# Kernel optimization log

Measured on AMD Instinct MI355X. Metric: run time of the kernel, lower is better.

The kernel has to match this reference:

```python
import jax, jax.numpy as jnp
import numpy as np
from jax import lax

VOCAB = 28996  # bert-base-cased vocab size (static for segment_sum)
B, S, D = 32, 512, 768
NUM_CLASSES = 9


def _lstm_dir(x, w_ih, w_hh, b_ih, b_hh):
    # x: [T, N, In]; torch gate order i, f, g, o packed along dim 0 of weights
    T, N, _ = x.shape
    H = w_hh.shape[1]
    xg = jnp.einsum('tni,gi->tng', x, w_ih) + b_ih  # precompute input projections [T,N,4H]

    def step(carry, xg_t):
        h, c = carry
        g = xg_t + h @ w_hh.T + b_hh
        i, f, gg, o = jnp.split(g, 4, axis=-1)
        c = jax.nn.sigmoid(f) * c + jax.nn.sigmoid(i) * jnp.tanh(gg)
        h = jax.nn.sigmoid(o) * jnp.tanh(c)
        return (h, c), h

    h0 = jnp.zeros((N, H), x.dtype)
    _, ys = lax.scan(step, (h0, h0), xg)
    return ys  # [T, N, H]


def setup_inputs() -> dict:
    key = jax.random.key(0)
    ks = jax.random.split(key, 8)
    H, In = D, 2 * D
    w = 0.02
    return {
        'batch': jax.random.randint(ks[0], (B, S), 0, VOCAB),
        'hidden': jax.random.normal(ks[1], (B, S, D), jnp.float32),
        'w_ih_f': jax.random.normal(ks[2], (4 * H, In), jnp.float32) * w,
        'w_hh_f': jax.random.normal(ks[3], (4 * H, H), jnp.float32) * w,
        'b_ih_f': jnp.zeros((4 * H,), jnp.float32),
        'b_hh_f': jnp.zeros((4 * H,), jnp.float32),
        'w_ih_b': jax.random.normal(ks[4], (4 * H, In), jnp.float32) * w,
        'w_hh_b': jax.random.normal(ks[5], (4 * H, H), jnp.float32) * w,
        'b_ih_b': jnp.zeros((4 * H,), jnp.float32),
        'b_hh_b': jnp.zeros((4 * H,), jnp.float32),
        'lin_w': jax.random.normal(ks[6], (NUM_CLASSES, 2 * H), jnp.float32) * w,
        'lin_b': jnp.zeros((NUM_CLASSES,), jnp.float32),
    }


def reference(batch, hidden, w_ih_f, w_hh_f, b_ih_f, b_hh_f,
              w_ih_b, w_hh_b, b_ih_b, b_hh_b, lin_w, lin_b):
    b, s, d = hidden.shape
    flat_ids = batch.reshape(-1)            # [B*S]
    flat_h = hidden.reshape(-1, d)          # [B*S, D]
    # segment mean of embeddings grouped by raw token id (the dict loop in torch)
    sums = jax.ops.segment_sum(flat_h, flat_ids, num_segments=VOCAB)
    counts = jax.ops.segment_sum(jnp.ones((flat_ids.shape[0], 1), hidden.dtype),
                                 flat_ids, num_segments=VOCAB)
    means = sums / jnp.maximum(counts, 1.0)
    ctx = means[flat_ids].reshape(b, s, d)  # gather-broadcast back per position
    x = jnp.concatenate([hidden, ctx], axis=2)  # [B, S, 2D]
    # nn.LSTM is not batch_first: scans over dim0 (B acts as time, S as batch)
    out_f = _lstm_dir(x, w_ih_f, w_hh_f, b_ih_f, b_hh_f)
    out_b = _lstm_dir(x[::-1], w_ih_b, w_hh_b, b_ih_b, b_hh_b)[::-1]
    out = jnp.concatenate([out_f, out_b], axis=-1)  # [B, S, 2D]
    # dropout is identity in eval mode
    return out @ lin_w.T + lin_b  # [B, S, num_classes]
```

## Files before the change

### kernel.cpp

```cpp
#include <hip/hip_runtime.h>

#define VOCAB 28996
#define BB 32
#define SS 512
#define DD 768
#define NCLS 9
#define ROWS (BB*SS)
#define IN2 (2*DD)
#define G4 (4*DD)
#define NB2 (2*G4)

typedef __attribute__((ext_vector_type(8))) short short8;
typedef __attribute__((ext_vector_type(4))) short shortx4;
typedef __attribute__((ext_vector_type(4))) float floatx4;
typedef unsigned long long ull;

__device__ __forceinline__ float bf2f(unsigned short u){
  union { unsigned int i; float f; } v; v.i = ((unsigned int)u) << 16; return v.f;
}
__device__ __forceinline__ unsigned short f2bf(float f){
  union { float f; unsigned int i; } v; v.f = f;
  unsigned int r = v.i + 0x7FFFu + ((v.i >> 16) & 1u);
  return (unsigned short)(r >> 16);
}
__device__ __forceinline__ float sigf(float x){ return 1.0f / (1.0f + __expf(-x)); }
__device__ __forceinline__ float tanhfast(float x){
  float y = fminf(fmaxf(x, -15.f), 15.f);
  float e = __expf(2.f * y);
  return 1.f - 2.f / (e + 1.f);
}

__device__ __forceinline__ void gl_lds16(const unsigned short* g, unsigned short* l){
  __builtin_amdgcn_global_load_lds((__attribute__((address_space(1))) void*)(g),
                                   (__attribute__((address_space(3))) void*)(l), 16, 0, 0);
}
__device__ __forceinline__ void gl_lds16_c(const unsigned short* g, unsigned short* l){
  __builtin_amdgcn_global_load_lds((__attribute__((address_space(1))) void*)(g),
                                   (__attribute__((address_space(3))) void*)(l), 16, 0, 17);
}
__device__ __forceinline__ void store16_sc1(unsigned short* p, short8 v){
  asm volatile("global_store_dwordx4 %0, %1, off sc0 sc1" :: "v"(p), "v"(v) : "memory");
}

__device__ __forceinline__ void grid_bar(unsigned* bar, int nb)
{
  __syncthreads();
  if (threadIdx.x == 0) {
    unsigned g = __hip_atomic_load(bar + 1, __ATOMIC_RELAXED, __HIP_MEMORY_SCOPE_AGENT);
    unsigned a = __hip_atomic_fetch_add(bar, 1u, __ATOMIC_RELAXED, __HIP_MEMORY_SCOPE_AGENT);
    if (a == (unsigned)(nb - 1)) {
      __hip_atomic_store(bar, 0u, __ATOMIC_RELAXED, __HIP_MEMORY_SCOPE_AGENT);
      __hip_atomic_store(bar + 1, g + 1u, __ATOMIC_RELEASE, __HIP_MEMORY_SCOPE_AGENT);
    } else {
      unsigned cur;
      do {
        __builtin_amdgcn_s_sleep(2);
        cur = __hip_atomic_load(bar + 1, __ATOMIC_RELAXED, __HIP_MEMORY_SCOPE_AGENT);
      } while (cur == g);
    }
  }
  __syncthreads();
}

__global__ void seg_scatter(const int* __restrict__ ids, const float* __restrict__ hidden,
                            float* __restrict__ sums, float* __restrict__ counts)
{
  int r = blockIdx.x;
  int id = ids[r];
  const float* h = hidden + (long)r * DD;
  float* s = sums + (long)id * DD;
  for (int d = threadIdx.x; d < DD; d += 256)
    atomicAdd(&s[d], h[d]);
  if (threadIdx.x == 0) atomicAdd(&counts[id], 1.0f);
}

__global__ void build_x(const int* __restrict__ ids, const float* __restrict__ hidden,
                        const float* __restrict__ sums, const float* __restrict__ counts,
                        unsigned short* __restrict__ x)
{
  int r = blockIdx.x;
  int id = ids[r];
  float inv = 1.0f / fmaxf(counts[id], 1.0f);
  const float* h = hidden + (long)r * DD;
  const float* s = sums + (long)id * DD;
  unsigned short* xr = x + (long)r * IN2;
  for (int d = threadIdx.x; d < DD; d += 256) {
    xr[d]      = f2bf(h[d]);
    xr[DD + d] = f2bf(s[d] * inv);
  }
}

__global__ void conv_w_perm(const float* __restrict__ w, unsigned short* __restrict__ o, int K)
{
  long i = (long)blockIdx.x * 256 + threadIdx.x;
  if (i >= (long)G4 * K) return;
  int row = (int)(i / K); int k = (int)(i - (long)row * K);
  int u = row >> 2, g = row & 3;
  o[i] = f2bf(w[((long)(g * DD + u)) * K + k]);
}

__global__ void conv_bias_perm(const float* __restrict__ bif, const float* __restrict__ bhf,
                               const float* __restrict__ bib, const float* __restrict__ bhb,
                               float* __restrict__ o)
{
  int n = blockIdx.x * 256 + threadIdx.x;
  if (n >= NB2) return;
  int d = n / G4, rr = n - d * G4, u = rr >> 2, g = rr & 3;
  int s = g * DD + u;
  o[n] = d ? (bib[s] + bhb[s]) : (bif[s] + bhf[s]);
}

__global__ __launch_bounds__(256, 2)
void gemm_bt(const unsigned short* __restrict__ A, int lda,
             const unsigned short* __restrict__ B, int ldb,
             unsigned short* __restrict__ C, int ldc,
             const float* __restrict__ bias, int K)
{
  __shared__ unsigned short lA[128 * 32];
  __shared__ unsigned short lB[128 * 32];
  const int t = threadIdx.x;
  const int lane = t & 63;
  const int wv = t >> 6;
  const int wm = wv >> 1, wn = wv & 1;
  const int l15 = lane & 15, q = lane >> 4;
  const long m0 = (long)blockIdx.y * 128;
  const long n0 = (long)blockIdx.x * 128;
  const int rowS = t >> 2;
  const int kc = (((t & 3) ^ ((t >> 3) & 3))) * 8;
  const int qsw = (q ^ ((l15 >> 1) & 3)) * 8;
  const unsigned short* gA = A + (m0 + rowS) * lda + kc;
  const unsigned short* gB = B + (n0 + rowS) * ldb + kc;
  unsigned short* dA0 = lA + (wv << 9);
  unsigned short* dA1 = lA + 2048 + (wv << 9);
  unsigned short* dB0 = lB + (wv << 9);
  unsigned short* dB1 = lB + 2048 + (wv << 9);

  floatx4 acc[4][4];
  #pragma unroll
  for (int i = 0; i < 4; i++)
    #pragma unroll
    for (int j = 0; j < 4; j++)
      acc[i][j] = (floatx4){0.f, 0.f, 0.f, 0.f};

  const long a64 = (long)64 * lda;
  const long b64 = (long)64 * ldb;
  for (int kt = 0; kt < K; kt += 32) {
    gl_lds16(gA + kt,       dA0);
    gl_lds16(gA + a64 + kt, dA1);
    gl_lds16(gB + kt,       dB0);
    gl_lds16(gB + b64 + kt, dB1);
    __syncthreads();
    short8 af[4], bfr[4];
    #pragma unroll
    for (int i = 0; i < 4; i++)
      af[i] = *(const short8*)(lA + (wm * 64 + i * 16 + l15) * 32 + qsw);
    #pragma unroll
    for (int j = 0; j < 4; j++)
      bfr[j] = *(const short8*)(lB + (wn * 64 + j * 16 + l15) * 32 + qsw);
    #pragma unroll
    for (int i = 0; i < 4; i++)
      #pragma unroll
      for (int j = 0; j < 4; j++)
        acc[i][j] = __builtin_amdgcn_mfma_f32_16x16x32_bf16(af[i], bfr[j], acc[i][j], 0, 0, 0);
    __syncthreads();
  }

  #pragma unroll
  for (int i = 0; i < 4; i++) {
    #pragma unroll
    for (int j = 0; j < 4; j++) {
      const long mg = m0 + wm * 64 + i * 16 + q * 4;
      const long ng = n0 + wn * 64 + j * 16 + l15;
      const float bb = bias[ng];
      #pragma unroll
      for (int r = 0; r < 4; r++)
        C[(mg + r) * ldc + ng] = f2bf(acc[i][j][r] + bb);
    }
  }
}

__global__ __launch_bounds__(512, 1)
void lstm_persist(const unsigned short* __restrict__ xg, int ldxg,
                  const unsigned short* __restrict__ whh,
                  unsigned short* __restrict__ hbuf,
                  unsigned short* __restrict__ outc,
                  unsigned* bar,
                  int dir0, int ndir)
{
  __shared__ unsigned short bufA[16384];
  __shared__ unsigned short bufB[16384];
  __shared__ unsigned short xgs[2][16384];
  __shared__ unsigned short hout[128 * 40];

  const int bid = blockIdx.x;
  const int xcd = bid & 7;
  const int idx = bid >> 3;
  int dm, k3;
  if (ndir == 2) { dm = idx & 7; k3 = idx >> 3; }
  else           { dm = idx & 3; k3 = idx >> 2; }
  const int ld  = (ndir == 2) ? (dm & 1) : 0;
  const int dir = dir0 + ld;
  const int mt  = (ndir == 2) ? (dm >> 1) : dm;
  const int nt  = k3 * 8 + xcd;
  const int m0 = mt * 128, n0 = nt * 128;
  const int u0 = n0 >> 2;
  unsigned* gbar = bar + dm * 16;

  const int t0 = threadIdx.x;
  const int lane = t0 & 63;
  const int wv = t0 >> 6;
  const int wm = wv >> 1;
  const int wn = wv & 1;
  const int l15 = lane & 15, q = lane >> 4;
  const long ldoff = (ndir == 2 && ld == 1) ? (long)G4 : 0;

  const unsigned short* Bdir = whh + (long)dir * G4 * DD;
  const int srow  = lane >> 2;
  const int scolA = (((lane & 3) ^ ((lane >> 3) & 3))) * 8;
  const int qsw   = (q ^ ((l15 >> 1) & 3)) * 8;
  const int xsw   = l15 << 3;
  const int xsrc  = (((t0 & 15) ^ ((t0 >> 4) & 15))) * 8;

  float c_reg[2][4];
  #pragma unroll
  for (int i = 0; i < 2; i++)
    #pragma unroll
    for (int j = 0; j < 4; j++)
      c_reg[i][j] = 0.f;

  {
    const int tt0 = dir ? (BB - 1) : 0;
    const unsigned short* xrow = xg + ((long)tt0 * SS + m0) * ldxg + ldoff + n0;
    #pragma unroll
    for (int c = 0; c < 4; c++) {
      int row = c * 32 + (t0 >> 4);
      gl_lds16(xrow + (long)row * ldxg + xsrc,
               xgs[0] + c * 4096 + (t0 >> 4) * 128 + (t0 & 15) * 8);
    }
  }

  for (int s = 0; s < BB; s++) {
    const int tt = dir ? (BB - 1 - s) : s;
    const unsigned short* hRead = hbuf + (((long)(s & 1)) * ndir + ld) * ((long)SS * DD);
    unsigned short* hw = hbuf + (((long)((s + 1) & 1)) * ndir + ld) * ((long)SS * DD);
    const unsigned short* xcur = xgs[s & 1];

    floatx4 acc[2][4];
    #pragma unroll
    for (int i = 0; i < 2; i++)
      #pragma unroll
      for (int j = 0; j < 4; j++)
        acc[i][j] = (floatx4){0.f, 0.f, 0.f, 0.f};

    for (int kt = 0; kt < 6; kt++) {
      const int kb = kt << 7;
      const int rb = wv * 16 + srow;
      #pragma unroll
      for (int p = 0; p < 4; p++) {
        gl_lds16_c(hRead + (long)(m0 + rb) * DD + kb + p * 32 + scolA,
                   bufA + p * 4096 + wv * 512 + lane * 8);
        gl_lds16(Bdir + (long)(n0 + rb) * DD + kb + p * 32 + scolA,
                 bufB + p * 4096 + wv * 512 + lane * 8);
      }
      __syncthreads();
      #pragma unroll
      for (int ks = 0; ks < 4; ks++) {
        short8 af[2], bfr[4];
        #pragma unroll
        for (int i = 0; i < 2; i++)
          af[i] = *(const short8*)(bufA + ks * 4096 + (wm * 32 + i * 16 + l15) * 32 + qsw);
        #pragma unroll
        for (int j = 0; j < 4; j++)
          bfr[j] = *(const short8*)(bufB + ks * 4096 + (wn * 64 + j * 16 + l15) * 32 + qsw);
        #pragma unroll
        for (int i = 0; i < 2; i++)
          #pragma unroll
          for (int j = 0; j < 4; j++)
            acc[i][j] = __builtin_amdgcn_mfma_f32_16x16x32_bf16(bfr[j], af[i], acc[i][j], 0, 0, 0);
      }
      __syncthreads();
    }

    #pragma unroll
    for (int i = 0; i < 2; i++) {
      const int mrow = wm * 32 + i * 16 + l15;
      const int xbase = mrow * 128;
      #pragma unroll
      for (int j = 0; j < 4; j++) {
        const int nb = wn * 64 + j * 16 + q * 4;
        shortx4 xv = *(const shortx4*)(xcur + xbase + (nb ^ xsw));
        float gi = acc[i][j][0] + bf2f((unsigned short)xv[0]);
        float gf = acc[i][j][1] + bf2f((unsigned short)xv[1]);
        float gg = acc[i][j][2] + bf2f((unsigned short)xv[2]);
        float go = acc[i][j][3] + bf2f((unsigned short)xv[3]);
        float c = sigf(gf) * c_reg[i][j] + sigf(gi) * tanhfast(gg);
        float h = sigf(go) * tanhfast(c);
        c_reg[i][j] = c;
        hout[mrow * 40 + (nb >> 2)] = f2bf(h);
      }
    }
    __syncthreads();
    {
      const int row = t0 >> 2;
      const int qq = t0 & 3;
      short8 v0 = *(const short8*)(hout + row * 40 + qq * 8);
      unsigned short* hwp = hw + (long)(m0 + row) * DD + u0 + qq * 8;
      unsigned short* op  = outc + ((long)tt * SS + m0 + row) * IN2 + dir * DD + u0 + qq * 8;
      store16_sc1(hwp, v0);
      *(short8*)op = v0;
    }
    asm volatile("s_waitcnt vmcnt(0)" ::: "memory");
    if (s < BB - 1) {
      const int tn = dir ? (BB - 2 - s) : (s + 1);
      const unsigned short* xrow = xg + ((long)tn * SS + m0) * ldxg + ldoff + n0;
      unsigned short* xnxt = xgs[(s + 1) & 1];
      #pragma unroll
      for (int c = 0; c < 4; c++) {
        int row = c * 32 + (t0 >> 4);
        gl_lds16(xrow + (long)row * ldxg + xsrc,
                 xnxt + c * 4096 + (t0 >> 4) * 128 + (t0 & 15) * 8);
      }
      grid_bar(gbar, 24);
    }
  }
}

__global__ void final_linear(const unsigned short* __restrict__ xin, const float* __restrict__ w,
                             const float* __restrict__ b, float* __restrict__ out)
{
  __shared__ float red[NCLS * 256];
  int row = blockIdx.x;
  const unsigned short* x = xin + (long)row * IN2;
  float p[NCLS];
  #pragma unroll
  for (int c = 0; c < NCLS; c++) p[c] = 0.f;
  for (int k = threadIdx.x; k < IN2; k += 256) {
    float xv = bf2f(x[k]);
    #pragma unroll
    for (int c = 0; c < NCLS; c++) p[c] += xv * w[c * IN2 + k];
  }
  #pragma unroll
  for (int c = 0; c < NCLS; c++) red[c * 256 + threadIdx.x] = p[c];
  __syncthreads();
  for (int s = 128; s > 0; s >>= 1) {
    if (threadIdx.x < s) {
      #pragma unroll
      for (int c = 0; c < NCLS; c++)
        red[c * 256 + threadIdx.x] += red[c * 256 + threadIdx.x + s];
    }
    __syncthreads();
  }
  if (threadIdx.x < NCLS)
    out[(long)row * NCLS + threadIdx.x] = red[threadIdx.x * 256] + b[threadIdx.x];
}

extern "C" void kernel_launch(void* const* d_in, const int* in_sizes, int n_in,
                              void* d_out, int out_size, void* d_ws, size_t ws_size,
                              hipStream_t stream)
{
  const int*   batch  = (const int*)d_in[0];
  const float* hidden = (const float*)d_in[1];
  const float* w_ih_f = (const float*)d_in[2];
  const float* w_hh_f = (const float*)d_in[3];
  const float* b_ih_f = (const float*)d_in[4];
  const float* b_hh_f = (const float*)d_in[5];
  const float* w_ih_b = (const float*)d_in[6];
  const float* w_hh_b = (const float*)d_in[7];
  const float* b_ih_b = (const float*)d_in[8];
  const float* b_hh_b = (const float*)d_in[9];
  const float* lin_w  = (const float*)d_in[10];
  const float* lin_b  = (const float*)d_in[11];
  float* out = (float*)d_out;

  char* ws = (char*)d_ws;
  size_t off = 0;
  auto alloc = [&](size_t bytes) -> char* {
    char* p = ws + off;
    off += (bytes + 255) & ~(size_t)255;
    return p;
  };

  const size_t SZ_XG_A = (size_t)ROWS * NB2 * 2;
  const size_t SZ_XG_B = (size_t)ROWS * G4  * 2;
  const size_t SZ_XBF  = (size_t)ROWS * IN2 * 2;
  const size_t SZ_W    = (size_t)G4 * IN2 * 2;
  const size_t SZ_BIAS = (size_t)NB2 * 4;
  const size_t SZ_HBUF = (size_t)2 * 2 * SS * DD * 2;
  const size_t SZ_BAR  = 512;
  const size_t SZ_SUMS = (size_t)VOCAB * DD * 4 + (size_t)VOCAB * 4;

  const size_t NEED_C = SZ_XG_A + SZ_XBF + SZ_W + SZ_BIAS + SZ_HBUF + SZ_BAR + 8 * 256;
  const bool combined = ws_size >= NEED_C;

  const long nWIH = (long)G4 * IN2;
  const long nWHH = (long)G4 * DD;

  if (combined) {
    unsigned short* xg   = (unsigned short*)alloc(SZ_XG_A);
    unsigned short* xbf  = (unsigned short*)alloc(SZ_XBF);
    unsigned short* wbuf = (unsigned short*)alloc(SZ_W);
    float*          bias = (float*)alloc(SZ_BIAS);
    unsigned short* hbuf = (unsigned short*)alloc(SZ_HBUF);
    unsigned*       bar  = (unsigned*)alloc(SZ_BAR);
    float* sums   = (float*)xg;
    float* counts = sums + (size_t)VOCAB * DD;

    hipMemsetAsync(sums, 0, SZ_SUMS, stream);
    hipMemsetAsync(bar, 0, SZ_BAR, stream);
    seg_scatter<<<ROWS, 256, 0, stream>>>(batch, hidden, sums, counts);
    build_x<<<ROWS, 256, 0, stream>>>(batch, hidden, sums, counts, xbf);
    conv_bias_perm<<<(NB2 + 255) / 256, 256, 0, stream>>>(b_ih_f, b_hh_f, b_ih_b, b_hh_b, bias);

    for (int dir = 0; dir < 2; dir++) {
      conv_w_perm<<<(unsigned)((nWIH + 255) / 256), 256, 0, stream>>>(dir ? w_ih_b : w_ih_f, wbuf, IN2);
      dim3 grid(G4 / 128, ROWS / 128, 1);
      gemm_bt<<<grid, 256, 0, stream>>>(xbf, IN2, wbuf, IN2,
                                        xg + (size_t)dir * G4, NB2,
                                        bias + (size_t)dir * G4, IN2);
    }
    conv_w_perm<<<(unsigned)((nWHH + 255) / 256), 256, 0, stream>>>(w_hh_f, wbuf, DD);
    conv_w_perm<<<(unsigned)((nWHH + 255) / 256), 256, 0, stream>>>(w_hh_b, wbuf + (size_t)G4 * DD, DD);

    hipMemsetAsync(hbuf, 0, SZ_HBUF, stream);
    lstm_persist<<<192, 512, 0, stream>>>(xg, NB2, wbuf, hbuf, xbf, bar, 0, 2);
    final_linear<<<ROWS, 256, 0, stream>>>(xbf, lin_w, lin_b, out);
  } else {
    unsigned short* xg   = (unsigned short*)alloc(SZ_XG_B);
    unsigned short* xbf  = (unsigned short*)alloc(SZ_XBF);
    unsigned short* outc = (unsigned short*)alloc(SZ_XBF);
    unsigned short* wih  = (unsigned short*)alloc(SZ_W);
    unsigned short* whh  = (unsigned short*)alloc(SZ_W);
    float*          bias = (float*)alloc(SZ_BIAS);
    unsigned short* hbuf = (unsigned short*)alloc(SZ_HBUF);
    unsigned*       bar  = (unsigned*)alloc(SZ_BAR);
    float* sums   = (float*)xg;
    float* counts = sums + (size_t)VOCAB * DD;

    hipMemsetAsync(sums, 0, SZ_SUMS, stream);
    hipMemsetAsync(bar, 0, SZ_BAR, stream);
    seg_scatter<<<ROWS, 256, 0, stream>>>(batch, hidden, sums, counts);
    build_x<<<ROWS, 256, 0, stream>>>(batch, hidden, sums, counts, xbf);
    conv_bias_perm<<<(NB2 + 255) / 256, 256, 0, stream>>>(b_ih_f, b_hh_f, b_ih_b, b_hh_b, bias);
    conv_w_perm<<<(unsigned)((nWHH + 255) / 256), 256, 0, stream>>>(w_hh_f, whh, DD);
    conv_w_perm<<<(unsigned)((nWHH + 255) / 256), 256, 0, stream>>>(w_hh_b, whh + (size_t)G4 * DD, DD);

    for (int dir = 0; dir < 2; dir++) {
      conv_w_perm<<<(unsigned)((nWIH + 255) / 256), 256, 0, stream>>>(dir ? w_ih_b : w_ih_f, wih, IN2);
      {
        dim3 grid(G4 / 128, ROWS / 128, 1);
        gemm_bt<<<grid, 256, 0, stream>>>(xbf, IN2, wih, IN2, xg, G4,
                                          bias + (size_t)dir * G4, IN2);
      }
      hipMemsetAsync(hbuf, 0, SZ_HBUF, stream);
      lstm_persist<<<96, 512, 0, stream>>>(xg, G4, whh, hbuf, outc, bar, dir, 1);
    }
    final_linear<<<ROWS, 256, 0, stream>>>(outc, lin_w, lin_b, out);
  }
}
```

Baseline: 1.251 ms.

## Double-buffer recurrent GEMM K-tiles and prefetch next x-gates before compute

The recurrent h@W_hh loop now uses 64-wide K tiles double-buffered in LDS. The next tile's global-to-LDS loads are issued while the current tile is in MFMA, with explicit vmcnt waits and raw s_barrier in place of __syncthreads. The next step's input-gate prefetch moves to the start of each step so it overlaps the GEMM rather than sitting on the critical path before the grid barrier. This adds more barriers and relies on hand-tuned vmcnt counts being correct, which risks subtle races if the counts are wrong.

```diff
diff --git a/kernel.cpp b/kernel.cpp
--- a/kernel.cpp
+++ b/kernel.cpp
@@ -42,25 +42,8 @@
   asm volatile("global_store_dwordx4 %0, %1, off sc0 sc1" :: "v"(p), "v"(v) : "memory");
 }
 
-__device__ __forceinline__ void grid_bar(unsigned* bar, int nb)
-{
-  __syncthreads();
-  if (threadIdx.x == 0) {
-    unsigned g = __hip_atomic_load(bar + 1, __ATOMIC_RELAXED, __HIP_MEMORY_SCOPE_AGENT);
-    unsigned a = __hip_atomic_fetch_add(bar, 1u, __ATOMIC_RELAXED, __HIP_MEMORY_SCOPE_AGENT);
-    if (a == (unsigned)(nb - 1)) {
-      __hip_atomic_store(bar, 0u, __ATOMIC_RELAXED, __HIP_MEMORY_SCOPE_AGENT);
-      __hip_atomic_store(bar + 1, g + 1u, __ATOMIC_RELEASE, __HIP_MEMORY_SCOPE_AGENT);
-    } else {
-      unsigned cur;
-      do {
-        __builtin_amdgcn_s_sleep(2);
-        cur = __hip_atomic_load(bar + 1, __ATOMIC_RELAXED, __HIP_MEMORY_SCOPE_AGENT);
-      } while (cur == g);
-    }
-  }
-  __syncthreads();
-}
+#define VMCNT(n) do { asm volatile("s_waitcnt vmcnt(" #n ")" ::: "memory"); \
+                      __builtin_amdgcn_sched_barrier(0); } while (0)
 
 __global__ void seg_scatter(const int* __restrict__ ids, const float* __restrict__ hidden,
                             float* __restrict__ sums, float* __restrict__ counts)
@@ -205,6 +188,7 @@
   const int m0 = mt * 128, n0 = nt * 128;
   const int u0 = n0 >> 2;
   unsigned* gbar = bar + dm * 16;
+  const int nb24 = 24;
 
   const int t0 = threadIdx.x;
   const int lane = t0 & 63;
@@ -221,6 +205,13 @@
   const int xsw   = l15 << 3;
   const int xsrc  = (((t0 & 15) ^ ((t0 >> 4) & 15))) * 8;
 
+  const int rb = wv * 16 + srow;
+  const unsigned short* wB  = Bdir + (long)(n0 + rb) * DD + scolA;
+  const unsigned short* hA0 = hbuf + ((long)0 * ndir + ld) * ((long)SS * DD) + (long)(m0 + rb) * DD + scolA;
+  const unsigned short* hA1 = hbuf + ((long)1 * ndir + ld) * ((long)SS * DD) + (long)(m0 + rb) * DD + scolA;
+  unsigned short* dstA = bufA + wv * 512 + lane * 8;
+  unsigned short* dstB = bufB + wv * 512 + lane * 8;
+
   float c_reg[2][4];
   #pragma unroll
   for (int i = 0; i < 2; i++)
@@ -241,10 +232,34 @@
 
   for (int s = 0; s < BB; s++) {
     const int tt = dir ? (BB - 1 - s) : s;
-    const unsigned short* hRead = hbuf + (((long)(s & 1)) * ndir + ld) * ((long)SS * DD);
+    const unsigned short* hA = (s & 1) ? hA1 : hA0;
     unsigned short* hw = hbuf + (((long)((s + 1) & 1)) * ndir + ld) * ((long)SS * DD);
     const unsigned short* xcur = xgs[s & 1];
 
+    {
+      gl_lds16_c(hA,        dstA);
+      gl_lds16_c(hA + 32,   dstA + 4096);
+      gl_lds16 (wB,         dstB);
+      gl_lds16 (wB + 32,    dstB + 4096);
+      gl_lds16_c(hA + 64,   dstA + 8192);
+      gl_lds16_c(hA + 96,   dstA + 12288);
+      gl_lds16 (wB + 64,    dstB + 8192);
+      gl_lds16 (wB + 96,    dstB + 12288);
+      if (s < BB - 1) {
+        const int tn = dir ? (BB - 2 - s) : (s + 1);
+        const unsigned short* xrow = xg + ((long)tn * SS + m0) * ldxg + ldoff + n0;
+        unsigned short* xnxt = xgs[(s + 1) & 1];
+        #pragma unroll
+        for (int c = 0; c < 4; c++) {
+          int row = c * 32 + (t0 >> 4);
+          gl_lds16(xrow + (long)row * ldxg + xsrc,
+                   xnxt + c * 4096 + (t0 >> 4) * 128 + (t0 & 15) * 8);
+        }
+      }
+    }
+    VMCNT(8);
+    __builtin_amdgcn_s_barrier();
+
     floatx4 acc[2][4];
     #pragma unroll
     for (int i = 0; i < 2; i++)
@@ -252,33 +267,41 @@
       for (int j = 0; j < 4; j++)
         acc[i][j] = (floatx4){0.f, 0.f, 0.f, 0.f};
 
-    for (int kt = 0; kt < 6; kt++) {
-      const int kb = kt << 7;
-      const int rb = wv * 16 + srow;
-      #pragma unroll
-      for (int p = 0; p < 4; p++) {
-        gl_lds16_c(hRead + (long)(m0 + rb) * DD + kb + p * 32 + scolA,
-                   bufA + p * 4096 + wv * 512 + lane * 8);
-        gl_lds16(Bdir + (long)(n0 + rb) * DD + kb + p * 32 + scolA,
-                 bufB + p * 4096 + wv * 512 + lane * 8);
-      }
-      __syncthreads();
-      #pragma unroll
-      for (int ks = 0; ks < 4; ks++) {
+    #pragma unroll
+    for (int kt = 0; kt < 12; kt++) {
+      const int cur = kt & 1;
+      const unsigned short* pA = bufA + cur * 8192;
+      const unsigned short* pB = bufB + cur * 8192;
+      #pragma unroll
+      for (int ks = 0; ks < 2; ks++) {
         short8 af[2], bfr[4];
         #pragma unroll
         for (int i = 0; i < 2; i++)
-          af[i] = *(const short8*)(bufA + ks * 4096 + (wm * 32 + i * 16 + l15) * 32 + qsw);
+          af[i] = *(const short8*)(pA + ks * 4096 + (wm * 32 + i * 16 + l15) * 32 + qsw);
         #pragma unroll
         for (int j = 0; j < 4; j++)
-          bfr[j] = *(const short8*)(bufB + ks * 4096 + (wn * 64 + j * 16 + l15) * 32 + qsw);
+          bfr[j] = *(const short8*)(pB + ks * 4096 + (wn * 64 + j * 16 + l15) * 32 + qsw);
         #pragma unroll
         for (int i = 0; i < 2; i++)
           #pragma unroll
           for (int j = 0; j < 4; j++)
             acc[i][j] = __builtin_amdgcn_mfma_f32_16x16x32_bf16(bfr[j], af[i], acc[i][j], 0, 0, 0);
       }
-      __syncthreads();
+      __builtin_amdgcn_s_barrier();
+      if (kt < 10) {
+        const long kb = (long)(kt + 2) * 64;
+        unsigned short* dA = bufA + cur * 8192 + wv * 512 + lane * 8;
+        unsigned short* dB = bufB + cur * 8192 + wv * 512 + lane * 8;
+        gl_lds16_c(hA + kb,      dA);
+        gl_lds16_c(hA + kb + 32, dA + 4096);
+        gl_lds16 (wB + kb,      dB);
+        gl_lds16 (wB + kb + 32, dB + 4096);
+        VMCNT(4);
+        __builtin_amdgcn_s_barrier();
+      } else if (kt == 10) {
+        VMCNT(0);
+        __builtin_amdgcn_s_barrier();
+      }
     }
 
     #pragma unroll
@@ -309,18 +332,24 @@
       store16_sc1(hwp, v0);
       *(short8*)op = v0;
     }
-    asm volatile("s_waitcnt vmcnt(0)" ::: "memory");
     if (s < BB - 1) {
-      const int tn = dir ? (BB - 2 - s) : (s + 1);
-      const unsigned short* xrow = xg + ((long)tn * SS + m0) * ldxg + ldoff + n0;
-      unsigned short* xnxt = xgs[(s + 1) & 1];
-      #pragma unroll
-      for (int c = 0; c < 4; c++) {
-        int row = c * 32 + (t0 >> 4);
-        gl_lds16(xrow + (long)row * ldxg + xsrc,
-                 xnxt + c * 4096 + (t0 >> 4) * 128 + (t0 & 15) * 8);
-      }
-      grid_bar(gbar, 24);
+      VMCNT(0);
+      __builtin_amdgcn_s_barrier();
+      if (threadIdx.x == 0) {
+        unsigned g = __hip_atomic_load(gbar + 1, __ATOMIC_RELAXED, __HIP_MEMORY_SCOPE_AGENT);
+        unsigned a = __hip_atomic_fetch_add(gbar, 1u, __ATOMIC_RELAXED, __HIP_MEMORY_SCOPE_AGENT);
+        if (a == (unsigned)(nb24 - 1)) {
+          __hip_atomic_store(gbar, 0u, __ATOMIC_RELAXED, __HIP_MEMORY_SCOPE_AGENT);
+          __hip_atomic_store(gbar + 1, g + 1u, __ATOMIC_RELEASE, __HIP_MEMORY_SCOPE_AGENT);
+        } else {
+          unsigned curv;
+          do {
+            __builtin_amdgcn_s_sleep(2);
+            curv = __hip_atomic_load(gbar + 1, __ATOMIC_RELAXED, __HIP_MEMORY_SCOPE_AGENT);
+          } while (curv == g);
+        }
+      }
+      __builtin_amdgcn_s_barrier();
     }
   }
 }
```

Measured after the change: 1.225 ms. 1.02x faster.
